# Performance work log

Measured on AMD Instinct MI355X. Metric: run time of the kernel, lower is better.

The kernel has to match this reference:

```python
import jax, jax.numpy as jnp
import numpy as np

V_TH = 1.0       # v_threshold
INIT_TAU = 2.0   # raw tau; decay = sigmoid(INIT_TAU)
T, B, IN_SZ, OUT_SZ = 32, 128, 2048, 2048


def setup_inputs() -> dict:
    key = jax.random.key(0)
    k1, k2 = jax.random.split(key)
    x = jax.random.normal(k1, (T, B, IN_SZ), jnp.float32)
    kernel = jax.random.normal(k2, (IN_SZ, OUT_SZ), jnp.float32) / np.sqrt(IN_SZ)
    return {"x": x, "kernel": kernel}


def reference(x, kernel):
    """Forward of Approx_OTPE's inner SNN step (f), scanned over time and
    vmapped over batch. Cell: u' = sigmoid(init_tau)*u + x @ W;
    s = heaviside(u' - v_th); soft reset u_out = u' - s*v_th.
    Returns stacked spikes [T, B, OUT_SZ]."""
    sig_tau = jax.nn.sigmoid(jnp.asarray(INIT_TAU, x.dtype))
    _, batch, _ = x.shape
    out_sz = kernel.shape[1]
    u0 = jnp.zeros((batch, out_sz), x.dtype)

    def body(u, xt):
        u_next = sig_tau * u + xt @ kernel          # [B, O]
        s = (u_next >= V_TH).astype(x.dtype)        # spike_fn forward
        u_out = u_next - s * V_TH                   # soft reset
        return u_out, s

    _, spikes = jax.lax.scan(body, u0, x)
    return spikes
```

## Files before the change

### kernel.cpp

```cpp
#include <hip/hip_runtime.h>
#include <math.h>
#include <stdint.h>

constexpr int T_STEPS = 32;
constexpr int BATCH   = 128;
constexpr int IN_SZ   = 2048;
constexpr int OUT_SZ  = 2048;


__device__ __forceinline__ void async_lds16(const float* gsrc, float* lds_dst) {
    __builtin_amdgcn_global_load_lds(
        (const __attribute__((address_space(1))) uint32_t*)(uintptr_t)gsrc,
        (__attribute__((address_space(3))) uint32_t*)(uint32_t)(uintptr_t)lds_dst,
        16, 0, 0);
}

__global__ __launch_bounds__(256, 4) void Approx_OTPE_67181878444197_kernel(
        const float* __restrict__ x,
        const float* __restrict__ W,
        float* __restrict__ out) {
    constexpr int BK = 16, BM = 128, BN = 64, BB = 4;
    constexpr int ASZ  = BK * BM;
    constexpr int BSZ  = BK * BN;
    constexpr int BUF  = ASZ + BSZ;
    constexpr int YSTR = BN + 1;
    constexpr int YSZ  = BM * YSTR;
    constexpr int NIT  = IN_SZ / BK;

    __shared__ float smem[YSZ];

    const int o0  = blockIdx.x * BN;
    const int b0  = blockIdx.y * BB;
    const int tid = threadIdx.x;
    const int ty  = tid >> 4;
    const int tx  = tid & 15;
    const int wv  = tid >> 6;

    const int am = tid >> 1;
    const int ak = (tid & 1) * 8;
    const int at = am >> 2;
    const int ab = am & 3;
    const size_t aBase = ((size_t)at * BATCH + (size_t)(b0 + ab)) * IN_SZ + ak;

    const int br = tid >> 4;
    const int bc = (tid & 15) * 4;

    float acc[8][4] = {};
    float su[8][4]  = {};

    {
        float* const A0 = smem;
        float* const B0 = smem + ASZ;
        async_lds16(&W[(size_t)br * OUT_SZ + o0 + bc], B0 + wv * 256);
        const float4 a0 = *reinterpret_cast<const float4*>(&x[aBase + 0]);
        const float4 a1 = *reinterpret_cast<const float4*>(&x[aBase + 4]);
        A0[(ak + 0) * BM + am] = a0.x;
        A0[(ak + 1) * BM + am] = a0.y;
        A0[(ak + 2) * BM + am] = a0.z;
        A0[(ak + 3) * BM + am] = a0.w;
        A0[(ak + 4) * BM + am] = a1.x;
        A0[(ak + 5) * BM + am] = a1.y;
        A0[(ak + 6) * BM + am] = a1.z;
        A0[(ak + 7) * BM + am] = a1.w;
    }
    __syncthreads();

    for (int it = 0; it < NIT; ++it) {
        const float* const Ac = smem + (it & 1) * BUF;
        const float* const Bc = Ac + ASZ;
        float* const An = smem + ((it + 1) & 1) * BUF;
        float* const Bn = An + ASZ;

        float4 pa0, pa1;
        const bool pre = (it < NIT - 1);
        if (pre) {
            const int k0n = (it + 1) * BK;
            async_lds16(&W[(size_t)(k0n + br) * OUT_SZ + o0 + bc], Bn + wv * 256);
            pa0 = *reinterpret_cast<const float4*>(&x[aBase + k0n]);
            pa1 = *reinterpret_cast<const float4*>(&x[aBase + k0n + 4]);
        }

        if (it == 32 || it == 64 || it == 96) {
            #pragma unroll
            for (int i = 0; i < 8; ++i)
                #pragma unroll
                for (int j = 0; j < 4; ++j) {
                    su[i][j]  = __fadd_rn(su[i][j], acc[i][j]);
                    acc[i][j] = 0.0f;
                }
        }

        #pragma unroll
        for (int k = 0; k < BK; ++k) {
            const float4 x0 = *reinterpret_cast<const float4*>(&Ac[k * BM + ty * 8]);
            const float4 x1 = *reinterpret_cast<const float4*>(&Ac[k * BM + ty * 8 + 4]);
            const float4 wf = *reinterpret_cast<const float4*>(&Bc[k * BN + tx * 4]);
            const float a[8] = {x0.x, x0.y, x0.z, x0.w, x1.x, x1.y, x1.z, x1.w};
            const float w[4] = {wf.x, wf.y, wf.z, wf.w};
            #pragma unroll
            for (int i = 0; i < 8; ++i)
                #pragma unroll
                for (int j = 0; j < 4; ++j)
                    acc[i][j] = __builtin_fmaf(a[i], w[j], acc[i][j]);
        }

        if (pre) {
            An[(ak + 0) * BM + am] = pa0.x;
            An[(ak + 1) * BM + am] = pa0.y;
            An[(ak + 2) * BM + am] = pa0.z;
            An[(ak + 3) * BM + am] = pa0.w;
            An[(ak + 4) * BM + am] = pa1.x;
            An[(ak + 5) * BM + am] = pa1.y;
            An[(ak + 6) * BM + am] = pa1.z;
            An[(ak + 7) * BM + am] = pa1.w;
        }
        __syncthreads();
    }

    #pragma unroll
    for (int i = 0; i < 8; ++i)
        #pragma unroll
        for (int j = 0; j < 4; ++j)
            smem[(ty * 8 + i) * YSTR + tx * 4 + j] = __fadd_rn(su[i][j], acc[i][j]);
    __syncthreads();

    {
        const int bl = tid >> 6;
        const int o  = tid & 63;
        const size_t plane  = (size_t)BATCH * OUT_SZ;
        const size_t outIdx = (size_t)(b0 + bl) * OUT_SZ + o0 + o;

        const double D = 1.0 / (1.0 + exp(-2.0));
        double u = 0.0;
        #pragma unroll
        for (int t = 0; t < T_STEPS; ++t) {
            const double y  = (double)smem[(t * 4 + bl) * YSTR + o];
            const double un = __dadd_rn(__dmul_rn(D, u), y);
            const double s  = (un >= 1.0) ? 1.0 : 0.0;
            u = __dsub_rn(un, s);
            out[(size_t)t * plane + outIdx] = (float)s;
        }
    }
}

extern "C" void kernel_launch(void* const* d_in, const int* in_sizes, int n_in,
                              void* d_out, int out_size, void* d_ws, size_t ws_size,
                              hipStream_t stream) {
    const float* x = (const float*)d_in[0];
    const float* W = (const float*)d_in[1];
    float* out     = (float*)d_out;

    dim3 grid(OUT_SZ / 64, BATCH / 4);
    Approx_OTPE_67181878444197_kernel<<<grid, 256, 0, stream>>>(x, W, out);
}
```

Measured before the change: 477.3 us.

## Halve block tile to 64 rows with 128 threads and two-phase epilogue

Each block shrinks from 256 threads covering 128 rows (32 timesteps x 4 batch) to 128 threads covering 64 rows (32 timesteps x 2 batch), doubling the grid. Each thread now issues two async W loads per K-step so the 16x64 W tile is still filled. The epilogue stages results through shared memory in two halves, because the smaller LDS buffer can no longer hold the full output tile. This gives more blocks and smaller LDS per block, but W is re-read by twice as many blocks, and launch bounds now allow only one block per CU.

```diff
diff --git a/kernel.cpp b/kernel.cpp
--- a/kernel.cpp
+++ b/kernel.cpp
@@ -15,22 +15,21 @@
         16, 0, 0);
 }
 
-__global__ __launch_bounds__(256, 4) void Approx_OTPE_67181878444197_kernel(
+__global__ __launch_bounds__(128, 1) void Approx_OTPE_67181878444197_kernel(
         const float* __restrict__ x,
         const float* __restrict__ W,
         float* __restrict__ out) {
-    constexpr int BK = 16, BM = 128, BN = 64, BB = 4;
-    constexpr int ASZ  = BK * BM;
-    constexpr int BSZ  = BK * BN;
-    constexpr int BUF  = ASZ + BSZ;
+    constexpr int BK = 16, BM = 64, BN = 64;
+    constexpr int ASZ = BK * BM;
+    constexpr int BSZ = BK * BN;
+    constexpr int BUF = ASZ + BSZ;
     constexpr int YSTR = BN + 1;
-    constexpr int YSZ  = BM * YSTR;
-    constexpr int NIT  = IN_SZ / BK;
+    constexpr int NIT = IN_SZ / BK;
 
-    __shared__ float smem[YSZ];
+    __shared__ float smem[2 * BUF];
 
     const int o0  = blockIdx.x * BN;
-    const int b0  = blockIdx.y * BB;
+    const int b0  = blockIdx.y * 2;
     const int tid = threadIdx.x;
     const int ty  = tid >> 4;
     const int tx  = tid & 15;
@@ -38,8 +37,8 @@
 
     const int am = tid >> 1;
     const int ak = (tid & 1) * 8;
-    const int at = am >> 2;
-    const int ab = am & 3;
+    const int at = am >> 1;
+    const int ab = am & 1;
     const size_t aBase = ((size_t)at * BATCH + (size_t)(b0 + ab)) * IN_SZ + ak;
 
     const int br = tid >> 4;
@@ -52,6 +51,7 @@
         float* const A0 = smem;
         float* const B0 = smem + ASZ;
         async_lds16(&W[(size_t)br * OUT_SZ + o0 + bc], B0 + wv * 256);
+        async_lds16(&W[(size_t)(8 + br) * OUT_SZ + o0 + bc], B0 + 512 + wv * 256);
         const float4 a0 = *reinterpret_cast<const float4*>(&x[aBase + 0]);
         const float4 a1 = *reinterpret_cast<const float4*>(&x[aBase + 4]);
         A0[(ak + 0) * BM + am] = a0.x;
@@ -65,6 +65,7 @@
     }
     __syncthreads();
 
+    #pragma unroll 1
     for (int it = 0; it < NIT; ++it) {
         const float* const Ac = smem + (it & 1) * BUF;
         const float* const Bc = Ac + ASZ;
@@ -75,7 +76,10 @@
         const bool pre = (it < NIT - 1);
         if (pre) {
             const int k0n = (it + 1) * BK;
-            async_lds16(&W[(size_t)(k0n + br) * OUT_SZ + o0 + bc], Bn + wv * 256);
+            async_lds16(&W[(size_t)(k0n + br) * OUT_SZ + o0 + bc],
+                        Bn + wv * 256);
+            async_lds16(&W[(size_t)(k0n + 8 + br) * OUT_SZ + o0 + bc],
+                        Bn + 512 + wv * 256);
             pa0 = *reinterpret_cast<const float4*>(&x[aBase + k0n]);
             pa1 = *reinterpret_cast<const float4*>(&x[aBase + k0n + 4]);
         }
@@ -121,20 +125,31 @@
     for (int i = 0; i < 8; ++i)
         #pragma unroll
         for (int j = 0; j < 4; ++j)
-            smem[(ty * 8 + i) * YSTR + tx * 4 + j] = __fadd_rn(su[i][j], acc[i][j]);
-    __syncthreads();
+            su[i][j] = __fadd_rn(su[i][j], acc[i][j]);
 
-    {
-        const int bl = tid >> 6;
-        const int o  = tid & 63;
-        const size_t plane  = (size_t)BATCH * OUT_SZ;
-        const size_t outIdx = (size_t)(b0 + bl) * OUT_SZ + o0 + o;
+    const int bl = tid >> 6;
+    const int o  = tid & 63;
+    const size_t plane  = (size_t)BATCH * OUT_SZ;
+    const size_t outIdx = (size_t)(b0 + bl) * OUT_SZ + o0 + o;
+    const double D = 1.0 / (1.0 + exp(-2.0));
+    double u = 0.0;
 
-        const double D = 1.0 / (1.0 + exp(-2.0));
-        double u = 0.0;
+    #pragma unroll
+    for (int p = 0; p < 2; ++p) {
+        __syncthreads();
+        if ((ty >> 2) == p) {
+            const int rb = ty * 8 - p * 32;
+            #pragma unroll
+            for (int i = 0; i < 8; ++i)
+                #pragma unroll
+                for (int j = 0; j < 4; ++j)
+                    smem[(rb + i) * YSTR + tx * 4 + j] = su[i][j];
+        }
+        __syncthreads();
         #pragma unroll
-        for (int t = 0; t < T_STEPS; ++t) {
-            const double y  = (double)smem[(t * 4 + bl) * YSTR + o];
+        for (int tt = 0; tt < 16; ++tt) {
+            const int t = p * 16 + tt;
+            const double y  = (double)smem[(tt * 2 + bl) * YSTR + o];
             const double un = __dadd_rn(__dmul_rn(D, u), y);
             const double s  = (un >= 1.0) ? 1.0 : 0.0;
             u = __dsub_rn(un, s);
@@ -150,6 +165,6 @@
     const float* W = (const float*)d_in[1];
     float* out     = (float*)d_out;
 
-    dim3 grid(OUT_SZ / 64, BATCH / 4);
-    Approx_OTPE_67181878444197_kernel<<<grid, 256, 0, stream>>>(x, W, out);
+    dim3 grid(OUT_SZ / 64, BATCH / 2);
+    Approx_OTPE_67181878444197_kernel<<<grid, 128, 0, stream>>>(x, W, out);
 }
```

Result: slower. 668.8 us (+40.1%).
